# Kernel optimization log

Hardware: AMD Instinct MI355X
Metric: run time of the kernel (lower is better)

## Reference

```python
import jax, jax.numpy as jnp
import numpy as np

TOP_K = 2
HORIZON = 10


def _lstm_layer(seq, w_ih, w_hh, b_ih, b_hh):
    """Single torch-style LSTM layer over seq [T, in]; returns hidden seq [T, hid]."""
    hid = w_hh.shape[1]
    def step(carry, x_t):
        h, c = carry
        z = x_t @ w_ih.T + h @ w_hh.T + b_ih + b_hh  # [4*hid], torch gate order i,f,g,o
        i, f, g, o = jnp.split(z, 4)
        c = jax.nn.sigmoid(f) * c + jax.nn.sigmoid(i) * jnp.tanh(g)
        h = jax.nn.sigmoid(o) * jnp.tanh(c)
        return (h, c), h
    init = (jnp.zeros((hid,), seq.dtype), jnp.zeros((hid,), seq.dtype))
    _, hs = jax.lax.scan(step, init, seq)
    return hs


def setup_inputs() -> dict:
    key = jax.random.key(0)
    ks = jax.random.split(key, 12)
    H, E = 4096, 64
    B, S = 4, 4096
    s = 0.02
    return {
        "x": jax.random.normal(ks[0], (B, S, H), jnp.float32),
        "gate_w": jax.random.normal(ks[1], (E, H), jnp.float32) * s,
        "expert_bias": jnp.zeros((E,), jnp.float32),
        "cp_w1": jax.random.normal(ks[2], (64, H), jnp.float32) * s,
        "cp_b1": jnp.zeros((64,), jnp.float32),
        "cp_w2": jax.random.normal(ks[3], (1, 64), jnp.float32) * s,
        "cp_b2": jnp.zeros((1,), jnp.float32),
        "load_buffer": jax.random.uniform(ks[4], (50, E), jnp.float32),
        "lp_w_ih0": jax.random.normal(ks[5], (256, E), jnp.float32) * s,
        "lp_w_hh0": jax.random.normal(ks[6], (256, 64), jnp.float32) * s,
        "lp_b_ih0": jnp.zeros((256,), jnp.float32),
        "lp_b_hh0": jnp.zeros((256,), jnp.float32),
        "lp_w_ih1": jax.random.normal(ks[7], (256, 64), jnp.float32) * s,
        "lp_w_hh1": jax.random.normal(ks[8], (256, 64), jnp.float32) * s,
        "lp_b_ih1": jnp.zeros((256,), jnp.float32),
        "lp_b_hh1": jnp.zeros((256,), jnp.float32),
        "head_w": jax.random.normal(ks[9], (E * HORIZON, 64), jnp.float32) * s,
        "head_b": jnp.zeros((E * HORIZON,), jnp.float32),
    }


def reference(x, gate_w, expert_bias, cp_w1, cp_b1, cp_w2, cp_b2, load_buffer,
              lp_w_ih0, lp_w_hh0, lp_b_ih0, lp_b_hh0,
              lp_w_ih1, lp_w_hh1, lp_b_ih1, lp_b_hh1, head_w, head_b):
    sg = jax.lax.stop_gradient
    B, S, H = x.shape
    E = gate_w.shape[0]
    flat = x.reshape(-1, H)                       # [N, H]
    N = flat.shape[0]

    # --- routing logits (small gate GEMM) ---
    logits = flat @ gate_w.T                      # [N, E]

    # --- LSTM load prediction (torch.no_grad in original) ---
    seq = sg(load_buffer)
    h1 = _lstm_layer(seq, sg(lp_w_ih0), sg(lp_w_hh0), sg(lp_b_ih0), sg(lp_b_hh0))
    h2 = _lstm_layer(h1, sg(lp_w_ih1), sg(lp_w_hh1), sg(lp_b_ih1), sg(lp_b_hh1))
    pred = h2[-1] @ sg(head_w).T + sg(head_b)     # [E*HORIZON]
    future_load = jax.nn.softmax(pred.reshape(E, HORIZON).mean(axis=1))  # [E]

    # --- bias + predicted-load adjustment, softmax, top-k ---
    adj_logits = logits + expert_bias - sg(future_load)
    probs = jax.nn.softmax(adj_logits, axis=-1)   # [N, E]
    top_scores, top_idx = jax.lax.top_k(probs, TOP_K)
    top_scores = top_scores / top_scores.sum(axis=-1, keepdims=True)

    # --- switch-style load-balancing auxiliary loss ---
    one_hot = jax.nn.one_hot(top_idx, E, dtype=probs.dtype)   # [N, k, E]
    f = one_hot.sum(axis=(0, 1)) / (N * TOP_K)                # routed fraction per expert
    P = probs.mean(axis=0)                                    # mean routing prob
    aux_loss = E * jnp.sum(f * P)

    # --- dynamic capacity from complexity predictor (torch.no_grad) ---
    comp = jax.nn.sigmoid(
        jax.nn.relu(flat @ sg(cp_w1).T + sg(cp_b1)) @ sg(cp_w2).T + sg(cp_b2))  # [N,1]
    capacity = jnp.clip(0.5 + 1.5 * comp.mean(), 0.5, 2.0)

    return top_scores, top_idx, aux_loss, capacity, future_load
```

## Files before the change

kernel.cpp:

```cpp
#include <hip/hip_runtime.h>
#include <stdint.h>

#define IMG_OFF_BYTES 80000
#define CHUNK_IMG 20480
#define LOGITS_OFF 680000
#define TAU 1e-3f

#define BUF_STRIDE 30720
#define BOFF 10240
#define XLOFF 5120
#define WLOFF 10240

typedef __attribute__((ext_vector_type(8))) short short8v;
typedef __attribute__((ext_vector_type(4))) short short4v;
typedef __attribute__((ext_vector_type(4))) float f32x4;

__device__ __forceinline__ float rlf(float v, int l) {
  return __int_as_float(__builtin_amdgcn_readlane(__float_as_int(v), l));
}
__device__ __forceinline__ float wsum(float v) {
#pragma unroll
  for (int o = 32; o; o >>= 1) v += __shfl_xor(v, o, 64);
  return v;
}
__device__ __forceinline__ float wmax(float v) {
#pragma unroll
  for (int o = 32; o; o >>= 1) v = fmaxf(v, __shfl_xor(v, o, 64));
  return v;
}
__device__ __forceinline__ unsigned short f2bf(float f) {
  unsigned u = __float_as_uint(f);
  u += 0x7fffu + ((u >> 16) & 1u);
  return (unsigned short)(u >> 16);
}
__device__ __forceinline__ float bf2f(unsigned short h) {
  return __uint_as_float(((unsigned)h) << 16);
}
__device__ __forceinline__ short8v frag8(const char* p0, const char* p1) {
  short4v a = *(const short4v*)p0;
  short4v b = *(const short4v*)p1;
  return __builtin_shufflevector(a, b, 0, 1, 2, 3, 4, 5, 6, 7);
}

__global__ __launch_bounds__(256) void prep_kernel(
    const float* __restrict__ gate_w, const float* __restrict__ cp_w1,
    float* __restrict__ ws)
{
  const int c = blockIdx.x;
  const int tid = threadIdx.x;
  if (c == 0 && tid < 144) ws[64 + tid] = 0.f;
  {
    float4 z = make_float4(0.f, 0.f, 0.f, 0.f);
    float4* lz = (float4*)(ws + LOGITS_OFF + c * 16384);
#pragma unroll
    for (int i = 0; i < 16; ++i) lz[tid + i * 256] = z;
  }
  const int row = tid >> 1;
  const int half = tid & 1;
  const float* src = (row < 64) ? (gate_w + (size_t)row * 4096)
                                : (cp_w1 + (size_t)(row - 64) * 4096);
  float v[16];
#pragma unroll
  for (int j = 0; j < 4; ++j)
    *(float4*)&v[j * 4] = *(const float4*)(src + c * 32 + half * 16 + j * 4);
  uint4 hv, lv;
  unsigned hu[8], lu[8];
#pragma unroll
  for (int i = 0; i < 8; ++i) {
    unsigned short h0 = f2bf(v[2 * i]), h1 = f2bf(v[2 * i + 1]);
    unsigned short l0 = f2bf(v[2 * i] - bf2f(h0));
    unsigned short l1 = f2bf(v[2 * i + 1] - bf2f(h1));
    hu[i] = (unsigned)h0 | ((unsigned)h1 << 16);
    lu[i] = (unsigned)l0 | ((unsigned)l1 << 16);
  }
  char* img = (char*)ws + IMG_OFF_BYTES + (size_t)c * CHUNK_IMG;
  hv.x = hu[0]; hv.y = hu[1]; hv.z = hu[2]; hv.w = hu[3];
  *(uint4*)(img + row * 80 + half * 32) = hv;
  hv.x = hu[4]; hv.y = hu[5]; hv.z = hu[6]; hv.w = hu[7];
  *(uint4*)(img + row * 80 + half * 32 + 16) = hv;
  lv.x = lu[0]; lv.y = lu[1]; lv.z = lu[2]; lv.w = lu[3];
  *(uint4*)(img + WLOFF + row * 80 + half * 32) = lv;
  lv.x = lu[4]; lv.y = lu[5]; lv.z = lu[6]; lv.w = lu[7];
  *(uint4*)(img + WLOFF + row * 80 + half * 32 + 16) = lv;
}

__device__ void lstm_device(
    char* ldsbase,
    const float* __restrict__ lb,
    const float* __restrict__ wih0, const float* __restrict__ whh0,
    const float* __restrict__ bih0, const float* __restrict__ bhh0,
    const float* __restrict__ wih1, const float* __restrict__ whh1,
    const float* __restrict__ bih1, const float* __restrict__ bhh1,
    const float* __restrict__ head_w, const float* __restrict__ head_b,
    float* __restrict__ ws, float* __restrict__ out, int N)
{
  float* seqh = (float*)ldsbase;
  float* h1s  = seqh + 3200;
  float* zbuf = h1s + 3200;
  float* hbuf = zbuf + 256;
  float* preds = hbuf + 64;
  const int tid = threadIdx.x;
  const int lane = tid & 63;
  for (int i = tid; i < 3200; i += 256) seqh[i] = lb[i];

  float hv = 0.f;
#pragma unroll 1
  for (int L = 0; L < 2; ++L) {
    const float* wip  = L ? wih1 : wih0;
    const float* whp  = L ? whh1 : whh0;
    const float* bip  = L ? bih1 : bih0;
    const float* bhp  = L ? bhh1 : bhh0;
    const float* seqp = L ? h1s  : seqh;
    float wiR[64], whR[64];
#pragma unroll
    for (int j = 0; j < 64; j += 4) {
      *(float4*)&wiR[j] = *(const float4*)(wip + tid * 64 + j);
      *(float4*)&whR[j] = *(const float4*)(whp + tid * 64 + j);
    }
    const float bsum = bip[tid] + bhp[tid];
    float c_reg = 0.f;
    hv = 0.f;
    if (tid < 64) hbuf[tid] = 0.f;
    __syncthreads();
#pragma unroll 1
    for (int t = 0; t < 50; ++t) {
      const float xv = seqp[t * 64 + lane];
      float a0 = bsum, a1 = 0.f, a2 = 0.f, a3 = 0.f;
#pragma unroll
      for (int j = 0; j < 64; j += 4) {
        a0 = fmaf(rlf(xv, j + 0), wiR[j + 0], a0);
        a1 = fmaf(rlf(xv, j + 1), wiR[j + 1], a1);
        a2 = fmaf(rlf(xv, j + 2), wiR[j + 2], a2);
        a3 = fmaf(rlf(xv, j + 3), wiR[j + 3], a3);
      }
#pragma unroll
      for (int j = 0; j < 64; j += 4) {
        a0 = fmaf(rlf(hv, j + 0), whR[j + 0], a0);
        a1 = fmaf(rlf(hv, j + 1), whR[j + 1], a1);
        a2 = fmaf(rlf(hv, j + 2), whR[j + 2], a2);
        a3 = fmaf(rlf(hv, j + 3), whR[j + 3], a3);
      }
      zbuf[tid] = (a0 + a1) + (a2 + a3);
      __syncthreads();
      if (tid < 64) {
        const float zi = zbuf[tid], zf = zbuf[64 + tid];
        const float zg = zbuf[128 + tid], zo = zbuf[192 + tid];
        const float si = 1.f / (1.f + expf(-zi));
        const float sf = 1.f / (1.f + expf(-zf));
        const float so = 1.f / (1.f + expf(-zo));
        c_reg = sf * c_reg + si * tanhf(zg);
        const float h = so * tanhf(c_reg);
        hbuf[tid] = h;
        if (L == 0) h1s[t * 64 + tid] = h;
      }
      __syncthreads();
      hv = hbuf[lane];
    }
    __syncthreads();
  }
  for (int o = tid; o < 640; o += 256) {
    const float* hw = head_w + o * 64;
    float a0 = 0.f, a1 = 0.f, a2 = 0.f, a3 = 0.f;
#pragma unroll
    for (int j = 0; j < 64; j += 4) {
      a0 = fmaf(rlf(hv, j + 0), hw[j + 0], a0);
      a1 = fmaf(rlf(hv, j + 1), hw[j + 1], a1);
      a2 = fmaf(rlf(hv, j + 2), hw[j + 2], a2);
      a3 = fmaf(rlf(hv, j + 3), hw[j + 3], a3);
    }
    preds[o] = (a0 + a1) + (a2 + a3) + head_b[o];
  }
  __syncthreads();
  if (tid < 64) {
    float m = 0.f;
#pragma unroll
    for (int h = 0; h < 10; ++h) m += preds[tid * 10 + h];
    m = m / 10.f;
    const float mx = wmax(m);
    const float p = expf(m - mx);
    const float s = wsum(p);
    const float flv = p / s;
    ws[tid] = flv;
    out[4 * N + 2 + tid] = flv;
  }
}

__global__ __launch_bounds__(256) void gemm_kernel(
    const float* __restrict__ x, float* __restrict__ ws, float* __restrict__ out,
    const float* __restrict__ lb,
    const float* __restrict__ wih0, const float* __restrict__ whh0,
    const float* __restrict__ bih0, const float* __restrict__ bhh0,
    const float* __restrict__ wih1, const float* __restrict__ whh1,
    const float* __restrict__ bih1, const float* __restrict__ bhh1,
    const float* __restrict__ head_w, const float* __restrict__ head_b,
    int N)
{
  __shared__ __align__(16) char lds[61440];
  if (blockIdx.x == 0) {
    lstm_device(lds, lb, wih0, whh0, bih0, bhh0, wih1, whh1, bih1, bhh1,
                head_w, head_b, ws, out, N);
    return;
  }
  const int b = blockIdx.x - 1;
  const int tb = (b & 255) * 64;
  const int ck0 = (b >> 8) * 64;
  const int tid = threadIdx.x;
  const int lane = tid & 63;
  const int wv = __builtin_amdgcn_readfirstlane(tid >> 6);
  const int r15 = lane & 15;
  const int fo = (lane >> 4) * 8;
  const int row = tid >> 2;
  const int kslot = tid & 3;
  const float* xsrc = x + (size_t)(tb + row) * 4096 + kslot * 8;
  const char* wimg = (const char*)ws + IMG_OFF_BYTES;
  char* buf0 = lds;
  char* buf1 = lds + BUF_STRIDE;

  f32x4 acc[4][2];
#pragma unroll
  for (int mi = 0; mi < 4; ++mi)
#pragma unroll
    for (int ni = 0; ni < 2; ++ni) acc[mi][ni] = (f32x4)0.f;

  float xa[8], xb[8];

#define LOADX(R, C)                                                        \
  { *(float4*)&R[0] = *(const float4*)(xsrc + (size_t)(C) * 32);           \
    *(float4*)&R[4] = *(const float4*)(xsrc + (size_t)(C) * 32 + 4); }

#define WRITEX(R, BASE)                                                    \
  { uint4 hv, lv; unsigned hu[4], lu[4];                                   \
    _Pragma("unroll")                                                      \
    for (int i = 0; i < 4; ++i) {                                          \
      unsigned short h0 = f2bf(R[2 * i]), h1 = f2bf(R[2 * i + 1]);         \
      unsigned short l0 = f2bf(R[2 * i] - bf2f(h0));                       \
      unsigned short l1 = f2bf(R[2 * i + 1] - bf2f(h1));                   \
      hu[i] = (unsigned)h0 | ((unsigned)h1 << 16);                         \
      lu[i] = (unsigned)l0 | ((unsigned)l1 << 16);                         \
    }                                                                      \
    hv.x = hu[0]; hv.y = hu[1]; hv.z = hu[2]; hv.w = hu[3];                \
    lv.x = lu[0]; lv.y = lu[1]; lv.z = lu[2]; lv.w = lu[3];                \
    *(uint4*)((BASE) + row * 80 + kslot * 16) = hv;                        \
    *(uint4*)((BASE) + XLOFF + row * 80 + kslot * 16) = lv; }

#define STAGEB(C, BASE)                                                    \
  { const char* s = wimg + (size_t)(C) * CHUNK_IMG + (wv * 5) * 1024 +     \
                    lane * 16;                                             \
    char* d = (BASE) + BOFF + (wv * 5) * 1024;                             \
    _Pragma("unroll")                                                      \
    for (int i = 0; i < 5; ++i)                                            \
      __builtin_amdgcn_global_load_lds(                                    \
          (const __attribute__((address_space(1))) uint32_t*)(s + i * 1024), \
          (__attribute__((address_space(3))) uint32_t*)(d + i * 1024),     \
          16, 0, 0); }

#define COMPUTE(BASE)                                                      \
  { const char* bA = (BASE);                                               \
    const char* bB = (BASE) + BOFF;                                        \
    short8v xh[4], xl[4], wh[2], wl[2];                                    \
    _Pragma("unroll")                                                      \
    for (int mi = 0; mi < 4; ++mi) {                                       \
      const char* p = bA + (mi * 16 + r15) * 80 + fo;                      \
      xh[mi] = frag8(p, p + 32);                                           \
      xl[mi] = frag8(p + XLOFF, p + XLOFF + 32);                           \
    }                                                                      \
    _Pragma("unroll")                                                      \
    for (int ni = 0; ni < 2; ++ni) {                                       \
      const char* p = bB + (wv * 32 + ni * 16 + r15) * 80 + fo;            \
      wh[ni] = frag8(p, p + 32);                                           \
      wl[ni] = frag8(p + WLOFF, p + WLOFF + 32);                           \
    }                                                                      \
    _Pragma("unroll")                                                      \
    for (int mi = 0; mi < 4; ++mi)                                         \
      _Pragma("unroll")                                                    \
      for (int ni = 0; ni < 2; ++ni) {                                     \
        acc[mi][ni] = __builtin_amdgcn_mfma_f32_16x16x32_bf16(             \
            xh[mi], wh[ni], acc[mi][ni], 0, 0, 0);                         \
        acc[mi][ni] = __builtin_amdgcn_mfma_f32_16x16x32_bf16(             \
            xh[mi], wl[ni], acc[mi][ni], 0, 0, 0);                         \
        acc[mi][ni] = __builtin_amdgcn_mfma_f32_16x16x32_bf16(             \
            xl[mi], wh[ni], acc[mi][ni], 0, 0, 0);                         \
      } }

  LOADX(xa, ck0);
  LOADX(xb, ck0 + 1);
  STAGEB(ck0, buf0);
  WRITEX(xa, buf0);
  __syncthreads();

#pragma unroll 1
  for (int cc = 0; cc < 32; ++cc) {
    const int c0 = ck0 + 2 * cc, c1 = c0 + 1;
    STAGEB(c0 + 1, buf1);
    if (cc < 31) LOADX(xa, c0 + 2);
    COMPUTE(buf0);
    WRITEX(xb, buf1);
    __syncthreads();
    if (cc < 31) STAGEB(c1 + 1, buf0);
    if (cc < 31) LOADX(xb, c1 + 2);
    COMPUTE(buf1);
    if (cc < 31) WRITEX(xa, buf0);
    __syncthreads();
  }

  float* lg = ws + LOGITS_OFF;
#pragma unroll
  for (int mi = 0; mi < 4; ++mi)
#pragma unroll
    for (int ni = 0; ni < 2; ++ni)
#pragma unroll
      for (int r = 0; r < 4; ++r) {
        const int tokrow = tb + mi * 16 + (lane >> 4) * 4 + r;
        const int col = wv * 32 + ni * 16 + r15;
        atomicAdd(&lg[(size_t)tokrow * 128 + col], acc[mi][ni][r]);
      }
#undef LOADX
#undef WRITEX
#undef STAGEB
#undef COMPUTE
}

__global__ __launch_bounds__(256) void epi_kernel(
    const float* __restrict__ eb_p, const float* __restrict__ cp_b1,
    const float* __restrict__ cp_w2, const float* __restrict__ cp_b2,
    float* __restrict__ ws, float* __restrict__ out, int N)
{
  const int tid = threadIdx.x;
  const int lane = tid & 63;
  const int wv = __builtin_amdgcn_readfirstlane(tid >> 6);
  const int tb = blockIdx.x * 32;
  const float* lg = ws + LOGITS_OFF;
  int* qd = (int*)(ws + 200);
  __shared__ float sP[64];
  __shared__ float scnt[64];
  __shared__ float scomp;
  if (tid < 64) { sP[tid] = 0.f; scnt[tid] = 0.f; }
  if (tid == 0) scomp = 0.f;
  __syncthreads();

  const float eb = eb_p[lane];
  const float fl = ws[lane];
  const float cb1 = cp_b1[lane];
  const float cw2 = cp_w2[lane];
  const float cb2 = cp_b2[0];
  float psum_local = 0.f, comp_local = 0.f;
  float* o_ts = out;
  float* o_ti = out + 2 * N;

#pragma unroll 1
  for (int tt = 0; tt < 8; ++tt) {
    const int tok = tb + wv * 8 + tt;
    const float lgv = lg[(size_t)tok * 128 + lane];
    const float lc  = lg[(size_t)tok * 128 + 64 + lane];
    float rr = fmaxf(lc + cb1, 0.f) * cw2;
    rr = wsum(rr);
    const float comp = 1.f / (1.f + expf(-(rr + cb2)));
    comp_local += comp;
    const float a = lgv + eb - fl;
    float m1 = a; int i1 = lane;
#pragma unroll
    for (int o = 32; o; o >>= 1) {
      const float ov = __shfl_xor(m1, o, 64);
      const int oi = __shfl_xor(i1, o, 64);
      if (ov > m1 || (ov == m1 && oi < i1)) { m1 = ov; i1 = oi; }
    }
    float m2 = (lane == i1) ? -1e30f : a; int i2 = lane;
#pragma unroll
    for (int o = 32; o; o >>= 1) {
      const float ov = __shfl_xor(m2, o, 64);
      const int oi = __shfl_xor(i2, o, 64);
      if (ov > m2 || (ov == m2 && oi < i2)) { m2 = ov; i2 = oi; }
    }
    float m3 = (lane == i1 || lane == i2) ? -1e30f : a;
#pragma unroll
    for (int o = 32; o; o >>= 1) m3 = fmaxf(m3, __shfl_xor(m3, o, 64));
    const float p = expf(a - m1);
    const float ssum = wsum(p);
    const float prob = p / ssum;
    psum_local += prob;
    const float s1 = rlf(prob, i1);
    const float s2 = rlf(prob, i2);
    if (lane == 0) {
      const float inv = 1.f / (s1 + s2);
      o_ts[tok * 2 + 0] = s1 * inv;
      o_ts[tok * 2 + 1] = s2 * inv;
      o_ti[tok * 2 + 0] = (float)i1;
      o_ti[tok * 2 + 1] = (float)i2;
      atomicAdd(&scnt[i1], 1.f);
      atomicAdd(&scnt[i2], 1.f);
      if (m1 - m2 < TAU || m2 - m3 < TAU) {
        int slot = atomicAdd(qd, 1);
        qd[8 + slot] = tok;
      }
    }
  }
  atomicAdd(&sP[lane], psum_local);
  if (lane == 0) atomicAdd(&scomp, comp_local);
  __syncthreads();
  if (tid < 64) {
    atomicAdd(&ws[64 + tid], sP[tid]);
    atomicAdd(&ws[128 + tid], scnt[tid]);
  }
  if (tid == 0) atomicAdd(&ws[192], scomp);
}

__global__ __launch_bounds__(256) void repair_kernel(
    const float* __restrict__ x, const float* __restrict__ gate_w,
    const float* __restrict__ eb_p, float* __restrict__ ws,
    float* __restrict__ out, int N)
{
  const int tid = threadIdx.x;
  __shared__ float red[256];
  int* qd = (int*)(ws + 200);
  const int qn = qd[0];
  float* o_ts = out;
  float* o_ti = out + 2 * N;

  for (int e = blockIdx.x; e < qn; e += gridDim.x) {
    const int tok = qd[8 + e];
    const int o = tid & 63;
    const int kq = tid >> 6;
    const float* xr = x + (size_t)tok * 4096 + kq * 1024;
    const float* wr = gate_w + (size_t)o * 4096 + kq * 1024;
    float s = 0.f;
#pragma unroll 4
    for (int j = 0; j < 256; ++j) {
      const float4 xv = *(const float4*)(xr + j * 4);
      const float4 wv = *(const float4*)(wr + j * 4);
      s = fmaf(xv.x, wv.x, s); s = fmaf(xv.y, wv.y, s);
      s = fmaf(xv.z, wv.z, s); s = fmaf(xv.w, wv.w, s);
    }
    red[tid] = s;
    __syncthreads();
    if (tid < 64) {
      const float a = red[tid] + red[64 + tid] + red[128 + tid] +
                      red[192 + tid] + eb_p[tid] - ws[tid];
      const int lane = tid;
      float m1 = a; int i1 = lane;
#pragma unroll
      for (int oo = 32; oo; oo >>= 1) {
        const float ov = __shfl_xor(m1, oo, 64);
        const int oi = __shfl_xor(i1, oo, 64);
        if (ov > m1 || (ov == m1 && oi < i1)) { m1 = ov; i1 = oi; }
      }
      float m2 = (lane == i1) ? -1e30f : a; int i2 = lane;
#pragma unroll
      for (int oo = 32; oo; oo >>= 1) {
        const float ov = __shfl_xor(m2, oo, 64);
        const int oi = __shfl_xor(i2, oo, 64);
        if (ov > m2 || (ov == m2 && oi < i2)) { m2 = ov; i2 = oi; }
      }
      const float p = expf(a - m1);
      const float ssum = wsum(p);
      const float s1 = rlf(p, i1) / ssum;
      const float s2 = rlf(p, i2) / ssum;
      if (lane == 0) {
        const int i1o = (int)o_ti[tok * 2 + 0];
        const int i2o = (int)o_ti[tok * 2 + 1];
        const float inv = 1.f / (s1 + s2);
        o_ts[tok * 2 + 0] = s1 * inv;
        o_ts[tok * 2 + 1] = s2 * inv;
        o_ti[tok * 2 + 0] = (float)i1;
        o_ti[tok * 2 + 1] = (float)i2;
        if (i1o != i1 || i2o != i2) {
          atomicAdd(&ws[128 + i1o], -1.f);
          atomicAdd(&ws[128 + i2o], -1.f);
          atomicAdd(&ws[128 + i1], 1.f);
          atomicAdd(&ws[128 + i2], 1.f);
        }
      }
    }
    __syncthreads();
  }
}

__global__ __launch_bounds__(64) void fin_kernel(const float* __restrict__ ws,
                                                 float* __restrict__ out, int N) {
  const int e = threadIdx.x;
  const float P = ws[64 + e] / (float)N;
  const float f = ws[128 + e] / (float)(2 * N);
  const float v = wsum(f * P);
  if (e == 0) {
    out[4 * N + 0] = 64.f * v;
    float cap = 0.5f + 1.5f * (ws[192] / (float)N);
    out[4 * N + 1] = fminf(fmaxf(cap, 0.5f), 2.f);
  }
}

extern "C" void kernel_launch(void* const* d_in, const int* in_sizes, int n_in,
                              void* d_out, int out_size, void* d_ws, size_t ws_size,
                              hipStream_t stream) {
  const float* x          = (const float*)d_in[0];
  const float* gate_w     = (const float*)d_in[1];
  const float* expert_bias= (const float*)d_in[2];
  const float* cp_w1      = (const float*)d_in[3];
  const float* cp_b1      = (const float*)d_in[4];
  const float* cp_w2      = (const float*)d_in[5];
  const float* cp_b2      = (const float*)d_in[6];
  const float* load_buffer= (const float*)d_in[7];
  const float* wih0       = (const float*)d_in[8];
  const float* whh0       = (const float*)d_in[9];
  const float* bih0       = (const float*)d_in[10];
  const float* bhh0       = (const float*)d_in[11];
  const float* wih1       = (const float*)d_in[12];
  const float* whh1       = (const float*)d_in[13];
  const float* bih1       = (const float*)d_in[14];
  const float* bhh1       = (const float*)d_in[15];
  const float* head_w     = (const float*)d_in[16];
  const float* head_b     = (const float*)d_in[17];
  float* out = (float*)d_out;
  float* ws  = (float*)d_ws;
  const int N = in_sizes[0] / 4096;

  prep_kernel<<<128, 256, 0, stream>>>(gate_w, cp_w1, ws);
  gemm_kernel<<<513, 256, 0, stream>>>(x, ws, out, load_buffer,
                                       wih0, whh0, bih0, bhh0,
                                       wih1, whh1, bih1, bhh1,
                                       head_w, head_b, N);
  epi_kernel<<<N / 32, 256, 0, stream>>>(expert_bias, cp_b1, cp_w2, cp_b2,
                                         ws, out, N);
  repair_kernel<<<128, 256, 0, stream>>>(x, gate_w, expert_bias, ws, out, N);
  fin_kernel<<<1, 64, 0, stream>>>(ws, out, N);
}
```

Baseline: 224.4 us.

## Prepack weights in MFMA fragment order and load them directly to registers

The prep kernel now writes the bf16 hi/lo weight image in per-lane MFMA fragment order. The GEMM kernel can then load weight fragments straight from global or L2 into registers, with no LDS staging. This removes half the LDS buffer, which allows more blocks per CU, and the K-split is doubled to 1025 blocks so each block handles 32 chunks instead of 64. The trade-off is more atomic adds into the logits buffer and weight loads on the critical path that LDS staging no longer hides.

```diff
diff --git a/kernel.cpp b/kernel.cpp
--- a/kernel.cpp
+++ b/kernel.cpp
@@ -2,14 +2,12 @@
 #include <stdint.h>
 
 #define IMG_OFF_BYTES 80000
-#define CHUNK_IMG 20480
+#define CHUNK_IMG 16384
 #define LOGITS_OFF 680000
 #define TAU 1e-3f
 
-#define BUF_STRIDE 30720
-#define BOFF 10240
 #define XLOFF 5120
-#define WLOFF 10240
+#define BUF_STRIDE 10240
 
 typedef __attribute__((ext_vector_type(8))) short short8v;
 typedef __attribute__((ext_vector_type(4))) short short4v;
@@ -57,31 +55,30 @@
   }
   const int row = tid >> 1;
   const int half = tid & 1;
-  const float* src = (row < 64) ? (gate_w + (size_t)row * 4096)
-                                : (cp_w1 + (size_t)(row - 64) * 4096);
+  const float* src = ((row < 64) ? (gate_w + (size_t)row * 4096)
+                                 : (cp_w1 + (size_t)(row - 64) * 4096)) + c * 32 + half * 16;
   float v[16];
 #pragma unroll
-  for (int j = 0; j < 4; ++j)
-    *(float4*)&v[j * 4] = *(const float4*)(src + c * 32 + half * 16 + j * 4);
-  uint4 hv, lv;
-  unsigned hu[8], lu[8];
-#pragma unroll
-  for (int i = 0; i < 8; ++i) {
-    unsigned short h0 = f2bf(v[2 * i]), h1 = f2bf(v[2 * i + 1]);
-    unsigned short l0 = f2bf(v[2 * i] - bf2f(h0));
-    unsigned short l1 = f2bf(v[2 * i + 1] - bf2f(h1));
-    hu[i] = (unsigned)h0 | ((unsigned)h1 << 16);
-    lu[i] = (unsigned)l0 | ((unsigned)l1 << 16);
-  }
-  char* img = (char*)ws + IMG_OFF_BYTES + (size_t)c * CHUNK_IMG;
-  hv.x = hu[0]; hv.y = hu[1]; hv.z = hu[2]; hv.w = hu[3];
-  *(uint4*)(img + row * 80 + half * 32) = hv;
-  hv.x = hu[4]; hv.y = hu[5]; hv.z = hu[6]; hv.w = hu[7];
-  *(uint4*)(img + row * 80 + half * 32 + 16) = hv;
-  lv.x = lu[0]; lv.y = lu[1]; lv.z = lu[2]; lv.w = lu[3];
-  *(uint4*)(img + WLOFF + row * 80 + half * 32) = lv;
-  lv.x = lu[4]; lv.y = lu[5]; lv.z = lu[6]; lv.w = lu[7];
-  *(uint4*)(img + WLOFF + row * 80 + half * 32 + 16) = lv;
+  for (int j = 0; j < 4; ++j) *(float4*)&v[j * 4] = *(const float4*)(src + j * 4);
+  const int g = row >> 4, r15 = row & 15;
+  char* img = (char*)ws + IMG_OFF_BYTES + (size_t)c * CHUNK_IMG + g * 2048;
+#pragma unroll
+  for (int q = 0; q < 4; ++q) {
+    unsigned short h0 = f2bf(v[4 * q + 0]), h1 = f2bf(v[4 * q + 1]);
+    unsigned short h2 = f2bf(v[4 * q + 2]), h3 = f2bf(v[4 * q + 3]);
+    unsigned short l0 = f2bf(v[4 * q + 0] - bf2f(h0));
+    unsigned short l1 = f2bf(v[4 * q + 1] - bf2f(h1));
+    unsigned short l2 = f2bf(v[4 * q + 2] - bf2f(h2));
+    unsigned short l3 = f2bf(v[4 * q + 3] - bf2f(h3));
+    uint2 hv, lv;
+    hv.x = (unsigned)h0 | ((unsigned)h1 << 16);
+    hv.y = (unsigned)h2 | ((unsigned)h3 << 16);
+    lv.x = (unsigned)l0 | ((unsigned)l1 << 16);
+    lv.y = (unsigned)l2 | ((unsigned)l3 << 16);
+    const int l = q * 16 + r15;
+    *(uint2*)(img + l * 16 + half * 8) = hv;
+    *(uint2*)(img + 1024 + l * 16 + half * 8) = lv;
+  }
 }
 
 __device__ void lstm_device(
@@ -195,7 +192,7 @@
     const float* __restrict__ head_w, const float* __restrict__ head_b,
     int N)
 {
-  __shared__ __align__(16) char lds[61440];
+  __shared__ __align__(16) char lds[30720];
   if (blockIdx.x == 0) {
     lstm_device(lds, lb, wih0, whh0, bih0, bhh0, wih1, whh1, bih1, bhh1,
                 head_w, head_b, ws, out, N);
@@ -203,7 +200,7 @@
   }
   const int b = blockIdx.x - 1;
   const int tb = (b & 255) * 64;
-  const int ck0 = (b >> 8) * 64;
+  const int ck0 = (b >> 8) * 32;
   const int tid = threadIdx.x;
   const int lane = tid & 63;
   const int wv = __builtin_amdgcn_readfirstlane(tid >> 6);
@@ -223,6 +220,7 @@
     for (int ni = 0; ni < 2; ++ni) acc[mi][ni] = (f32x4)0.f;
 
   float xa[8], xb[8];
+  short8v wh[2], wl[2];
 
 #define LOADX(R, C)                                                        \
   { *(float4*)&R[0] = *(const float4*)(xsrc + (size_t)(C) * 32);           \
@@ -243,32 +241,20 @@
     *(uint4*)((BASE) + row * 80 + kslot * 16) = hv;                        \
     *(uint4*)((BASE) + XLOFF + row * 80 + kslot * 16) = lv; }
 
-#define STAGEB(C, BASE)                                                    \
-  { const char* s = wimg + (size_t)(C) * CHUNK_IMG + (wv * 5) * 1024 +     \
-                    lane * 16;                                             \
-    char* d = (BASE) + BOFF + (wv * 5) * 1024;                             \
-    _Pragma("unroll")                                                      \
-    for (int i = 0; i < 5; ++i)                                            \
-      __builtin_amdgcn_global_load_lds(                                    \
-          (const __attribute__((address_space(1))) uint32_t*)(s + i * 1024), \
-          (__attribute__((address_space(3))) uint32_t*)(d + i * 1024),     \
-          16, 0, 0); }
+#define WLOAD(C)                                                           \
+  { const char* wb = wimg + (size_t)(C) * CHUNK_IMG + wv * 4096 + lane * 16; \
+    wh[0] = *(const short8v*)wb;                                           \
+    wl[0] = *(const short8v*)(wb + 1024);                                  \
+    wh[1] = *(const short8v*)(wb + 2048);                                  \
+    wl[1] = *(const short8v*)(wb + 3072); }
 
 #define COMPUTE(BASE)                                                      \
-  { const char* bA = (BASE);                                               \
-    const char* bB = (BASE) + BOFF;                                        \
-    short8v xh[4], xl[4], wh[2], wl[2];                                    \
+  { short8v xh[4], xl[4];                                                  \
     _Pragma("unroll")                                                      \
     for (int mi = 0; mi < 4; ++mi) {                                       \
-      const char* p = bA + (mi * 16 + r15) * 80 + fo;                      \
+      const char* p = (BASE) + (mi * 16 + r15) * 80 + fo;                  \
       xh[mi] = frag8(p, p + 32);                                           \
       xl[mi] = frag8(p + XLOFF, p + XLOFF + 32);                           \
-    }                                                                      \
-    _Pragma("unroll")                                                      \
-    for (int ni = 0; ni < 2; ++ni) {                                       \
-      const char* p = bB + (wv * 32 + ni * 16 + r15) * 80 + fo;            \
-      wh[ni] = frag8(p, p + 32);                                           \
-      wl[ni] = frag8(p + WLOFF, p + WLOFF + 32);                           \
     }                                                                      \
     _Pragma("unroll")                                                      \
     for (int mi = 0; mi < 4; ++mi)                                         \
@@ -284,22 +270,21 @@
 
   LOADX(xa, ck0);
   LOADX(xb, ck0 + 1);
-  STAGEB(ck0, buf0);
   WRITEX(xa, buf0);
   __syncthreads();
 
 #pragma unroll 1
-  for (int cc = 0; cc < 32; ++cc) {
+  for (int cc = 0; cc < 16; ++cc) {
     const int c0 = ck0 + 2 * cc, c1 = c0 + 1;
-    STAGEB(c0 + 1, buf1);
-    if (cc < 31) LOADX(xa, c0 + 2);
+    WLOAD(c0);
+    if (cc < 15) LOADX(xa, c0 + 2);
     COMPUTE(buf0);
     WRITEX(xb, buf1);
     __syncthreads();
-    if (cc < 31) STAGEB(c1 + 1, buf0);
-    if (cc < 31) LOADX(xb, c1 + 2);
+    WLOAD(c1);
+    if (cc < 15) LOADX(xb, c1 + 2);
     COMPUTE(buf1);
-    if (cc < 31) WRITEX(xa, buf0);
+    if (cc < 15) WRITEX(xa, buf0);
     __syncthreads();
   }
 
@@ -316,7 +301,7 @@
       }
 #undef LOADX
 #undef WRITEX
-#undef STAGEB
+#undef WLOAD
 #undef COMPUTE
 }
 
@@ -513,10 +498,10 @@
   const int N = in_sizes[0] / 4096;
 
   prep_kernel<<<128, 256, 0, stream>>>(gate_w, cp_w1, ws);
-  gemm_kernel<<<513, 256, 0, stream>>>(x, ws, out, load_buffer,
-                                       wih0, whh0, bih0, bhh0,
-                                       wih1, whh1, bih1, bhh1,
-                                       head_w, head_b, N);
+  gemm_kernel<<<1025, 256, 0, stream>>>(x, ws, out, load_buffer,
+                                        wih0, whh0, bih0, bhh0,
+                                        wih1, whh1, bih1, bhh1,
+                                        head_w, head_b, N);
   epi_kernel<<<N / 32, 256, 0, stream>>>(expert_bias, cp_b1, cp_w2, cp_b2,
                                          ws, out, N);
   repair_kernel<<<128, 256, 0, stream>>>(x, gate_w, expert_bias, ws, out, N);
```

Result: faster. 199.9 us (-10.9%).
